# Optimization experiments

Hardware: AMD Instinct MI355X
Metric: run time of the kernel (lower is better)

Reference implementation:

```python
import jax, jax.numpy as jnp
import numpy as np

N_NODES = 65536
N_EDGES = 1048576
IN_CH, HID_CH, OUT_CH = 300, 64, 20
DROPOUT_P = 0.5


def setup_inputs() -> dict:
    key = jax.random.key(0)
    ks = jax.random.split(key, 6)
    x = jax.random.normal(ks[0], (N_NODES, IN_CH), dtype=jnp.float32)
    edge_index = jax.random.randint(ks[1], (2, N_EDGES), 0, N_NODES, dtype=jnp.int64)
    edge_weight = jax.random.uniform(ks[2], (N_EDGES,), dtype=jnp.float32)
    # Glorot-ish init for linear weights (PyG lin has no bias; GCNConv adds its own bias)
    W1 = jax.random.normal(ks[3], (IN_CH, HID_CH), dtype=jnp.float32) / np.sqrt(IN_CH)
    b1 = jnp.zeros((HID_CH,), dtype=jnp.float32)
    W2 = jax.random.normal(ks[4], (HID_CH, OUT_CH), dtype=jnp.float32) / np.sqrt(HID_CH)
    b2 = jnp.zeros((OUT_CH,), dtype=jnp.float32)
    return {"x": x, "edge_index": edge_index, "edge_weight": edge_weight,
            "W1": W1, "b1": b1, "W2": W2, "b2": b2}


def _gcn_conv(x, src, dst, edge_weight, W, b, num_nodes):
    # GCNConv with add_self_loops=False, normalize=False:
    #   h = x @ W; out[i] = sum_{e: dst(e)=i} w_e * h[src(e)]; out += b
    h = x @ W                                   # [N, C_out]
    msg = h[src] * edge_weight[:, None]         # [E, C_out]
    agg = jax.ops.segment_sum(msg, dst, num_segments=num_nodes)
    return agg + b


def reference(x, edge_index, edge_weight, W1, b1, W2, b2):
    num_nodes = x.shape[0]
    src, dst = edge_index[0], edge_index[1]
    h = _gcn_conv(x, src, dst, edge_weight, W1, b1, num_nodes)
    h = jax.nn.relu(h)
    # dropout p=0.5, training=True, deterministic fixed key
    keep = jax.random.bernoulli(jax.random.key(42), 1.0 - DROPOUT_P, h.shape)
    h = jnp.where(keep, h / (1.0 - DROPOUT_P), 0.0)
    out = _gcn_conv(h, src, dst, edge_weight, W2, b2, num_nodes)
    return out
```

## Files before the change

kernel.cpp:

```cpp
#include <hip/hip_runtime.h>

#define N_NODES 65536
#define N_EDGES 1048576
#define NB 256
#define CAP 4608
#define EPB_A 4096
#define BLK_A (N_EDGES / EPB_A)
#define EPT_A (EPB_A / 256)

typedef __attribute__((ext_vector_type(8))) short short8v;
typedef __attribute__((ext_vector_type(4))) float float4v;

__device__ __forceinline__ unsigned short f2bf(float f) {
  unsigned u = __float_as_uint(f);
  unsigned r = u + 0x7FFFu + ((u >> 16) & 1u);
  return (unsigned short)(r >> 16);
}
__device__ __forceinline__ float bflo(unsigned u) { return __uint_as_float(u << 16); }
__device__ __forceinline__ float bfhi(unsigned u) { return __uint_as_float(u & 0xFFFF0000u); }

__device__ __forceinline__ bool keep_mask(unsigned idx) {
  const unsigned k0 = 0u, k1 = 42u;
  const unsigned k2 = 0x1BD11BDAu ^ k0 ^ k1;
  unsigned x0 = 0u;
  unsigned x1 = idx;
  x0 += k0; x1 += k1;
#define TF_ROUND(r) { x0 += x1; x1 = (x1 << (r)) | (x1 >> (32 - (r))); x1 ^= x0; }
  TF_ROUND(13) TF_ROUND(15) TF_ROUND(26) TF_ROUND(6)
  x0 += k1; x1 += k2 + 1u;
  TF_ROUND(17) TF_ROUND(29) TF_ROUND(16) TF_ROUND(24)
  x0 += k2; x1 += k0 + 2u;
  TF_ROUND(13) TF_ROUND(15) TF_ROUND(26) TF_ROUND(6)
  x0 += k0; x1 += k1 + 3u;
  TF_ROUND(17) TF_ROUND(29) TF_ROUND(16) TF_ROUND(24)
  x0 += k1; x1 += k2 + 4u;
  TF_ROUND(13) TF_ROUND(15) TF_ROUND(26) TF_ROUND(6)
  x0 += k2; x1 += k0 + 5u;
#undef TF_ROUND
  return ((x0 ^ x1) & 0x80000000u) == 0u;
}

__global__ __launch_bounds__(256) void prep_w1(const float* __restrict__ W1,
                                               unsigned short* __restrict__ Wt,
                                               unsigned* __restrict__ gcur) {
  if (blockIdx.x == 0) gcur[threadIdx.x] = 0u;
  int i = blockIdx.x * 256 + threadIdx.x;
  if (i >= 64 * 320) return;
  int ch = i / 320, k = i % 320;
  float v = (k < 300) ? W1[k * 64 + ch] : 0.0f;
  Wt[i] = f2bf(v);
}

__global__ __launch_bounds__(256) void bin_pass(const int* __restrict__ ei,
                                                const float* __restrict__ ew,
                                                unsigned* __restrict__ gcur,
                                                uint2* __restrict__ binned) {
  __shared__ unsigned cnt[NB], lofs[NB], lcur[NB], gbase[NB];
  __shared__ uint2 stage[EPB_A];
  const int t = threadIdx.x;
  const int e0 = blockIdx.x * EPB_A;
  cnt[t] = 0u;
  lcur[t] = 0u;
  __syncthreads();
  unsigned pk[EPT_A], pw[EPT_A];
#pragma unroll
  for (int j = 0; j < EPT_A; ++j) {
    int e = e0 + t + j * 256;
    unsigned s = (unsigned)ei[e];
    unsigned d = (unsigned)ei[N_EDGES + e];
    pk[j] = s | (d << 16);
    pw[j] = __float_as_uint(ew[e]);
    atomicAdd(&cnt[d >> 8], 1u);
  }
  __syncthreads();
  lofs[t] = cnt[t];
  __syncthreads();
  for (int d = 1; d < NB; d <<= 1) {
    unsigned u = (t >= d) ? lofs[t - d] : 0u;
    __syncthreads();
    lofs[t] += u;
    __syncthreads();
  }
  unsigned incl = lofs[t];
  lofs[t] = incl - cnt[t];
  gbase[t] = (unsigned)t * CAP + atomicAdd(&gcur[t], cnt[t]);
  __syncthreads();
#pragma unroll
  for (int j = 0; j < EPT_A; ++j) {
    unsigned b = pk[j] >> 24;
    unsigned slot = lofs[b] + atomicAdd(&lcur[b], 1u);
    stage[slot] = make_uint2(pk[j], pw[j]);
  }
  __syncthreads();
  for (int s = t; s < EPB_A; s += 256) {
    uint2 u = stage[s];
    unsigned b = u.x >> 24;
    binned[gbase[b] + ((unsigned)s - lofs[b])] = u;
  }
}

__global__ __launch_bounds__(256) void bucket_sort(const unsigned* __restrict__ gcur,
                                                   const uint2* __restrict__ binned,
                                                   unsigned* __restrict__ sortedc,
                                                   unsigned* __restrict__ offs_p) {
  __shared__ uint2 eLDS[CAP];
  __shared__ unsigned cnt[NB], cur[NB];
  const int t = threadIdx.x;
  const int b = blockIdx.x;
  const unsigned lo = (unsigned)b * CAP;
  const unsigned n_edges = gcur[b];
  cnt[t] = 0u;
  __syncthreads();
  for (unsigned i = t; i < n_edges; i += 256) {
    uint2 u = binned[lo + i];
    eLDS[i] = u;
    atomicAdd(&cnt[(u.x >> 16) & 255u], 1u);
  }
  __syncthreads();
  cur[t] = cnt[t];
  __syncthreads();
  for (int d = 1; d < NB; d <<= 1) {
    unsigned u = (t >= d) ? cur[t - d] : 0u;
    __syncthreads();
    cur[t] += u;
    __syncthreads();
  }
  unsigned excl = cur[t] - cnt[t];
  offs_p[b * NB + t] = (lo + excl) | (cnt[t] << 21);
  __syncthreads();
  cur[t] = excl;
  __syncthreads();
  for (unsigned i = t; i < n_edges; i += 256) {
    uint2 u = eLDS[i];
    unsigned lo8 = (u.x >> 16) & 255u;
    unsigned p = lo + atomicAdd(&cur[lo8], 1u);
    sortedc[p] = (u.x & 0xFFFFu) | ((unsigned)f2bf(__uint_as_float(u.y)) << 16);
  }
}

__global__ __launch_bounds__(256) void gemm1_mfma(const float* __restrict__ x,
                                                  const unsigned short* __restrict__ Wt,
                                                  unsigned short* __restrict__ h1b) {
  __shared__ unsigned short As[64][72];
  __shared__ unsigned short Bs[64][72];
  const int t = threadIdx.x;
  const int node0 = blockIdx.x * 64;
  const int wave = t >> 6, lane = t & 63;
  const int quad = lane >> 4, l16 = lane & 15;
  float4v acc[4] = {{0.f,0.f,0.f,0.f},{0.f,0.f,0.f,0.f},{0.f,0.f,0.f,0.f},{0.f,0.f,0.f,0.f}};

  for (int kt = 0; kt < 5; ++kt) {
    const int k0 = kt * 64;
    for (int f = t; f < 1024; f += 256) {
      int node = f >> 4;
      int k = (f & 15) * 4;
      uint2 packed;
      if (k0 + k < 300) {
        float4 v = *(const float4*)(x + (size_t)(node0 + node) * 300 + k0 + k);
        packed.x = (unsigned)f2bf(v.x) | ((unsigned)f2bf(v.y) << 16);
        packed.y = (unsigned)f2bf(v.z) | ((unsigned)f2bf(v.w) << 16);
      } else {
        packed.x = 0u; packed.y = 0u;
      }
      *(uint2*)&As[node][k] = packed;
    }
    for (int f = t; f < 512; f += 256) {
      int ch = f >> 3;
      int kq = f & 7;
      uint4 v = *(const uint4*)(Wt + (size_t)ch * 320 + k0 + kq * 8);
      *(uint4*)&Bs[ch][kq * 8] = v;
    }
    __syncthreads();
    short8v a0 = *(const short8v*)&As[wave * 16 + l16][quad * 8];
    short8v a1 = *(const short8v*)&As[wave * 16 + l16][32 + quad * 8];
#pragma unroll
    for (int nt = 0; nt < 4; ++nt) {
      short8v b0 = *(const short8v*)&Bs[nt * 16 + l16][quad * 8];
      short8v b1 = *(const short8v*)&Bs[nt * 16 + l16][32 + quad * 8];
      acc[nt] = __builtin_amdgcn_mfma_f32_16x16x32_bf16(a0, b0, acc[nt], 0, 0, 0);
      acc[nt] = __builtin_amdgcn_mfma_f32_16x16x32_bf16(a1, b1, acc[nt], 0, 0, 0);
    }
    __syncthreads();
  }
#pragma unroll
  for (int nt = 0; nt < 4; ++nt) {
#pragma unroll
    for (int r = 0; r < 4; ++r) {
      h1b[(size_t)(node0 + wave * 16 + quad * 4 + r) * 64 + nt * 16 + l16] = f2bf(acc[nt][r]);
    }
  }
}

__global__ __launch_bounds__(256) void agg1_gemm2(const unsigned* __restrict__ offs_p,
                                                  const unsigned* __restrict__ sortedc,
                                                  const unsigned short* __restrict__ h1b,
                                                  const float* __restrict__ b1,
                                                  const float* __restrict__ W2,
                                                  unsigned* __restrict__ g32u) {
  __shared__ float h2[16][68];
  __shared__ float w2t[20][68];
  const int t = threadIdx.x;
  const int node0 = blockIdx.x * 16;
  for (int i = t; i < 64 * 20; i += 256) {
    w2t[i % 20][i / 20] = W2[i];
  }
  const int n = t >> 4, cg = t & 15;
  const int node = node0 + n;
  const unsigned op = offs_p[node];
  const unsigned s = op & 0x1FFFFFu;
  const unsigned e_end = s + (op >> 21);
  float4 acc = *(const float4*)(b1 + cg * 4);
  unsigned i = s;
  for (; i + 8 <= e_end; i += 8) {
    unsigned e0 = sortedc[i],     e1 = sortedc[i + 1], e2 = sortedc[i + 2], e3 = sortedc[i + 3];
    unsigned e4 = sortedc[i + 4], e5 = sortedc[i + 5], e6 = sortedc[i + 6], e7 = sortedc[i + 7];
    uint2 v0 = *(const uint2*)(h1b + ((size_t)(e0 & 0xFFFFu)) * 64 + cg * 4);
    uint2 v1 = *(const uint2*)(h1b + ((size_t)(e1 & 0xFFFFu)) * 64 + cg * 4);
    uint2 v2 = *(const uint2*)(h1b + ((size_t)(e2 & 0xFFFFu)) * 64 + cg * 4);
    uint2 v3 = *(const uint2*)(h1b + ((size_t)(e3 & 0xFFFFu)) * 64 + cg * 4);
    uint2 v4 = *(const uint2*)(h1b + ((size_t)(e4 & 0xFFFFu)) * 64 + cg * 4);
    uint2 v5 = *(const uint2*)(h1b + ((size_t)(e5 & 0xFFFFu)) * 64 + cg * 4);
    uint2 v6 = *(const uint2*)(h1b + ((size_t)(e6 & 0xFFFFu)) * 64 + cg * 4);
    uint2 v7 = *(const uint2*)(h1b + ((size_t)(e7 & 0xFFFFu)) * 64 + cg * 4);
    float w0 = bfhi(e0), w1 = bfhi(e1), w2 = bfhi(e2), w3 = bfhi(e3);
    float w4 = bfhi(e4), w5 = bfhi(e5), w6 = bfhi(e6), w7 = bfhi(e7);
    acc.x = fmaf(w0, bflo(v0.x), acc.x); acc.y = fmaf(w0, bfhi(v0.x), acc.y);
    acc.z = fmaf(w0, bflo(v0.y), acc.z); acc.w = fmaf(w0, bfhi(v0.y), acc.w);
    acc.x = fmaf(w1, bflo(v1.x), acc.x); acc.y = fmaf(w1, bfhi(v1.x), acc.y);
    acc.z = fmaf(w1, bflo(v1.y), acc.z); acc.w = fmaf(w1, bfhi(v1.y), acc.w);
    acc.x = fmaf(w2, bflo(v2.x), acc.x); acc.y = fmaf(w2, bfhi(v2.x), acc.y);
    acc.z = fmaf(w2, bflo(v2.y), acc.z); acc.w = fmaf(w2, bfhi(v2.y), acc.w);
    acc.x = fmaf(w3, bflo(v3.x), acc.x); acc.y = fmaf(w3, bfhi(v3.x), acc.y);
    acc.z = fmaf(w3, bflo(v3.y), acc.z); acc.w = fmaf(w3, bfhi(v3.y), acc.w);
    acc.x = fmaf(w4, bflo(v4.x), acc.x); acc.y = fmaf(w4, bfhi(v4.x), acc.y);
    acc.z = fmaf(w4, bflo(v4.y), acc.z); acc.w = fmaf(w4, bfhi(v4.y), acc.w);
    acc.x = fmaf(w5, bflo(v5.x), acc.x); acc.y = fmaf(w5, bfhi(v5.x), acc.y);
    acc.z = fmaf(w5, bflo(v5.y), acc.z); acc.w = fmaf(w5, bfhi(v5.y), acc.w);
    acc.x = fmaf(w6, bflo(v6.x), acc.x); acc.y = fmaf(w6, bfhi(v6.x), acc.y);
    acc.z = fmaf(w6, bflo(v6.y), acc.z); acc.w = fmaf(w6, bfhi(v6.y), acc.w);
    acc.x = fmaf(w7, bflo(v7.x), acc.x); acc.y = fmaf(w7, bfhi(v7.x), acc.y);
    acc.z = fmaf(w7, bflo(v7.y), acc.z); acc.w = fmaf(w7, bfhi(v7.y), acc.w);
  }
  for (; i < e_end; ++i) {
    unsigned e0 = sortedc[i];
    uint2 v0 = *(const uint2*)(h1b + ((size_t)(e0 & 0xFFFFu)) * 64 + cg * 4);
    float w0 = bfhi(e0);
    acc.x = fmaf(w0, bflo(v0.x), acc.x); acc.y = fmaf(w0, bfhi(v0.x), acc.y);
    acc.z = fmaf(w0, bflo(v0.y), acc.z); acc.w = fmaf(w0, bfhi(v0.y), acc.w);
  }
  const unsigned gi = (unsigned)node * 64u + (unsigned)cg * 4u;
  float r[4] = {acc.x, acc.y, acc.z, acc.w};
#pragma unroll
  for (int j = 0; j < 4; ++j) {
    float v = fmaxf(r[j], 0.0f);
    h2[n][cg * 4 + j] = keep_mask(gi + j) ? v * 2.0f : 0.0f;
  }
  __syncthreads();
  float d0 = 0.0f, d1 = 0.0f;
  if (cg < 10) {
    const int c0 = cg * 2, c1 = cg * 2 + 1;
#pragma unroll
    for (int k = 0; k < 64; k += 4) {
      float4 hv = *(const float4*)(&h2[n][k]);
      float4 w0 = *(const float4*)(&w2t[c0][k]);
      float4 w1 = *(const float4*)(&w2t[c1][k]);
      d0 = fmaf(hv.x, w0.x, d0); d0 = fmaf(hv.y, w0.y, d0);
      d0 = fmaf(hv.z, w0.z, d0); d0 = fmaf(hv.w, w0.w, d0);
      d1 = fmaf(hv.x, w1.x, d1); d1 = fmaf(hv.y, w1.y, d1);
      d1 = fmaf(hv.z, w1.z, d1); d1 = fmaf(hv.w, w1.w, d1);
    }
  }
  unsigned packed = (cg < 10) ? ((unsigned)f2bf(d0) | ((unsigned)f2bf(d1) << 16)) : 0u;
  g32u[(size_t)node * 16 + cg] = packed;
}

__global__ __launch_bounds__(256) void aggregate2(const unsigned* __restrict__ offs_p,
                                                  const unsigned* __restrict__ sortedc,
                                                  const unsigned* __restrict__ g32u,
                                                  const float* __restrict__ b2,
                                                  float* __restrict__ out) {
  const int t = threadIdx.x;
  const int n = blockIdx.x * 16 + (t >> 4);
  const int cg = t & 15;
  const unsigned op = offs_p[n];
  const unsigned s = op & 0x1FFFFFu;
  const unsigned e_end = s + (op >> 21);
  float ax = 0.0f, ay = 0.0f;
  unsigned i = s;
  for (; i + 8 <= e_end; i += 8) {
    unsigned e0 = sortedc[i],     e1 = sortedc[i + 1], e2 = sortedc[i + 2], e3 = sortedc[i + 3];
    unsigned e4 = sortedc[i + 4], e5 = sortedc[i + 5], e6 = sortedc[i + 6], e7 = sortedc[i + 7];
    unsigned v0 = g32u[(size_t)(e0 & 0xFFFFu) * 16 + cg];
    unsigned v1 = g32u[(size_t)(e1 & 0xFFFFu) * 16 + cg];
    unsigned v2 = g32u[(size_t)(e2 & 0xFFFFu) * 16 + cg];
    unsigned v3 = g32u[(size_t)(e3 & 0xFFFFu) * 16 + cg];
    unsigned v4 = g32u[(size_t)(e4 & 0xFFFFu) * 16 + cg];
    unsigned v5 = g32u[(size_t)(e5 & 0xFFFFu) * 16 + cg];
    unsigned v6 = g32u[(size_t)(e6 & 0xFFFFu) * 16 + cg];
    unsigned v7 = g32u[(size_t)(e7 & 0xFFFFu) * 16 + cg];
    float w0 = bfhi(e0), w1 = bfhi(e1), w2 = bfhi(e2), w3 = bfhi(e3);
    float w4 = bfhi(e4), w5 = bfhi(e5), w6 = bfhi(e6), w7 = bfhi(e7);
    ax = fmaf(w0, bflo(v0), ax); ay = fmaf(w0, bfhi(v0), ay);
    ax = fmaf(w1, bflo(v1), ax); ay = fmaf(w1, bfhi(v1), ay);
    ax = fmaf(w2, bflo(v2), ax); ay = fmaf(w2, bfhi(v2), ay);
    ax = fmaf(w3, bflo(v3), ax); ay = fmaf(w3, bfhi(v3), ay);
    ax = fmaf(w4, bflo(v4), ax); ay = fmaf(w4, bfhi(v4), ay);
    ax = fmaf(w5, bflo(v5), ax); ay = fmaf(w5, bfhi(v5), ay);
    ax = fmaf(w6, bflo(v6), ax); ay = fmaf(w6, bfhi(v6), ay);
    ax = fmaf(w7, bflo(v7), ax); ay = fmaf(w7, bfhi(v7), ay);
  }
  for (; i < e_end; ++i) {
    unsigned e0 = sortedc[i];
    unsigned v0 = g32u[(size_t)(e0 & 0xFFFFu) * 16 + cg];
    float w0 = bfhi(e0);
    ax = fmaf(w0, bflo(v0), ax); ay = fmaf(w0, bfhi(v0), ay);
  }
  if (cg < 10) {
    float2 o = make_float2(ax + b2[cg * 2], ay + b2[cg * 2 + 1]);
    *(float2*)(out + (size_t)n * 20 + cg * 2) = o;
  }
}

extern "C" void kernel_launch(void* const* d_in, const int* in_sizes, int n_in,
                              void* d_out, int out_size, void* d_ws, size_t ws_size,
                              hipStream_t stream) {
  const float* x  = (const float*)d_in[0];
  const int*   ei = (const int*)d_in[1];
  const float* ew = (const float*)d_in[2];
  const float* W1 = (const float*)d_in[3];
  const float* b1 = (const float*)d_in[4];
  const float* W2 = (const float*)d_in[5];
  const float* b2 = (const float*)d_in[6];
  float* out = (float*)d_out;

  unsigned short* h1b     = (unsigned short*)d_ws;
  unsigned*       g32u    = (unsigned*)(h1b + (size_t)N_NODES * 64);
  uint2*          binned  = (uint2*)(g32u + (size_t)N_NODES * 16);
  unsigned*       sortedc = (unsigned*)(binned + (size_t)NB * CAP);
  unsigned*       offs_p  = sortedc + (size_t)NB * CAP;
  unsigned short* Wt      = (unsigned short*)(offs_p + N_NODES);
  unsigned*       gcur    = (unsigned*)(Wt + 64 * 320);

  prep_w1<<<(64 * 320 + 255) / 256, 256, 0, stream>>>(W1, Wt, gcur);
  bin_pass<<<BLK_A, 256, 0, stream>>>(ei, ew, gcur, binned);
  bucket_sort<<<NB, 256, 0, stream>>>(gcur, binned, sortedc, offs_p);
  gemm1_mfma<<<N_NODES / 64, 256, 0, stream>>>(x, Wt, h1b);
  agg1_gemm2<<<N_NODES / 16, 256, 0, stream>>>(offs_p, sortedc, h1b, b1, W2, g32u);
  aggregate2<<<N_NODES / 16, 256, 0, stream>>>(offs_p, sortedc, g32u, b2, out);
}
```

Before: 223.0 us.

## Merge bucket sort and GEMM1 into one launch; use nontemporal edge loads

Measured after the change: 232.4 us. 4.2% more time.

```diff
diff --git a/kernel.cpp b/kernel.cpp
--- a/kernel.cpp
+++ b/kernel.cpp
@@ -99,94 +99,106 @@
   }
 }
 
-__global__ __launch_bounds__(256) void bucket_sort(const unsigned* __restrict__ gcur,
-                                                   const uint2* __restrict__ binned,
-                                                   unsigned* __restrict__ sortedc,
-                                                   unsigned* __restrict__ offs_p) {
-  __shared__ uint2 eLDS[CAP];
-  __shared__ unsigned cnt[NB], cur[NB];
-  const int t = threadIdx.x;
-  const int b = blockIdx.x;
-  const unsigned lo = (unsigned)b * CAP;
-  const unsigned n_edges = gcur[b];
-  cnt[t] = 0u;
-  __syncthreads();
-  for (unsigned i = t; i < n_edges; i += 256) {
-    uint2 u = binned[lo + i];
-    eLDS[i] = u;
-    atomicAdd(&cnt[(u.x >> 16) & 255u], 1u);
-  }
-  __syncthreads();
-  cur[t] = cnt[t];
-  __syncthreads();
-  for (int d = 1; d < NB; d <<= 1) {
-    unsigned u = (t >= d) ? cur[t - d] : 0u;
-    __syncthreads();
-    cur[t] += u;
-    __syncthreads();
-  }
-  unsigned excl = cur[t] - cnt[t];
-  offs_p[b * NB + t] = (lo + excl) | (cnt[t] << 21);
-  __syncthreads();
-  cur[t] = excl;
-  __syncthreads();
-  for (unsigned i = t; i < n_edges; i += 256) {
-    uint2 u = eLDS[i];
-    unsigned lo8 = (u.x >> 16) & 255u;
-    unsigned p = lo + atomicAdd(&cur[lo8], 1u);
-    sortedc[p] = (u.x & 0xFFFFu) | ((unsigned)f2bf(__uint_as_float(u.y)) << 16);
-  }
-}
-
-__global__ __launch_bounds__(256) void gemm1_mfma(const float* __restrict__ x,
+union SortGemmLDS {
+  struct {
+    unsigned long long e[CAP];
+    unsigned cnt[NB], cur[NB];
+  } bs;
+  struct {
+    unsigned short As[64][72];
+    unsigned short Bs[64][72];
+  } g1;
+};
+
+__global__ __launch_bounds__(256) void sort_gemm1(const unsigned* __restrict__ gcur,
+                                                  const uint2* __restrict__ binned,
+                                                  unsigned* __restrict__ sortedc,
+                                                  unsigned* __restrict__ offs_p,
+                                                  const float* __restrict__ x,
                                                   const unsigned short* __restrict__ Wt,
                                                   unsigned short* __restrict__ h1b) {
-  __shared__ unsigned short As[64][72];
-  __shared__ unsigned short Bs[64][72];
+  __shared__ SortGemmLDS sh;
   const int t = threadIdx.x;
-  const int node0 = blockIdx.x * 64;
-  const int wave = t >> 6, lane = t & 63;
-  const int quad = lane >> 4, l16 = lane & 15;
-  float4v acc[4] = {{0.f,0.f,0.f,0.f},{0.f,0.f,0.f,0.f},{0.f,0.f,0.f,0.f},{0.f,0.f,0.f,0.f}};
-
-  for (int kt = 0; kt < 5; ++kt) {
-    const int k0 = kt * 64;
-    for (int f = t; f < 1024; f += 256) {
-      int node = f >> 4;
-      int k = (f & 15) * 4;
-      uint2 packed;
-      if (k0 + k < 300) {
-        float4 v = *(const float4*)(x + (size_t)(node0 + node) * 300 + k0 + k);
-        packed.x = (unsigned)f2bf(v.x) | ((unsigned)f2bf(v.y) << 16);
-        packed.y = (unsigned)f2bf(v.z) | ((unsigned)f2bf(v.w) << 16);
-      } else {
-        packed.x = 0u; packed.y = 0u;
+
+  if (blockIdx.x < NB) {
+    const int b = blockIdx.x;
+    const unsigned lo = (unsigned)b * CAP;
+    const unsigned n_edges = gcur[b];
+    const unsigned long long* bin64 = (const unsigned long long*)binned;
+    sh.bs.cnt[t] = 0u;
+    __syncthreads();
+    for (unsigned i = t; i < n_edges; i += 256) {
+      unsigned long long u = __builtin_nontemporal_load(&bin64[lo + i]);
+      sh.bs.e[i] = u;
+      atomicAdd(&sh.bs.cnt[((unsigned)u >> 16) & 255u], 1u);
+    }
+    __syncthreads();
+    sh.bs.cur[t] = sh.bs.cnt[t];
+    __syncthreads();
+    for (int d = 1; d < NB; d <<= 1) {
+      unsigned u = (t >= d) ? sh.bs.cur[t - d] : 0u;
+      __syncthreads();
+      sh.bs.cur[t] += u;
+      __syncthreads();
+    }
+    unsigned excl = sh.bs.cur[t] - sh.bs.cnt[t];
+    offs_p[b * NB + t] = (lo + excl) | (sh.bs.cnt[t] << 21);
+    __syncthreads();
+    sh.bs.cur[t] = excl;
+    __syncthreads();
+    for (unsigned i = t; i < n_edges; i += 256) {
+      unsigned long long u = sh.bs.e[i];
+      unsigned key = (unsigned)u;
+      unsigned wbits = (unsigned)(u >> 32);
+      unsigned lo8 = (key >> 16) & 255u;
+      unsigned p = lo + atomicAdd(&sh.bs.cur[lo8], 1u);
+      sortedc[p] = (key & 0xFFFFu) | ((unsigned)f2bf(__uint_as_float(wbits)) << 16);
+    }
+  } else {
+    const int node0 = (blockIdx.x - NB) * 64;
+    const int wave = t >> 6, lane = t & 63;
+    const int quad = lane >> 4, l16 = lane & 15;
+    float4v acc[4] = {{0.f,0.f,0.f,0.f},{0.f,0.f,0.f,0.f},{0.f,0.f,0.f,0.f},{0.f,0.f,0.f,0.f}};
+
+    for (int kt = 0; kt < 5; ++kt) {
+      const int k0 = kt * 64;
+      for (int f = t; f < 1024; f += 256) {
+        int node = f >> 4;
+        int k = (f & 15) * 4;
+        uint2 packed;
+        if (k0 + k < 300) {
+          float4 v = *(const float4*)(x + (size_t)(node0 + node) * 300 + k0 + k);
+          packed.x = (unsigned)f2bf(v.x) | ((unsigned)f2bf(v.y) << 16);
+          packed.y = (unsigned)f2bf(v.z) | ((unsigned)f2bf(v.w) << 16);
+        } else {
+          packed.x = 0u; packed.y = 0u;
+        }
+        *(uint2*)&sh.g1.As[node][k] = packed;
       }
-      *(uint2*)&As[node][k] = packed;
-    }
-    for (int f = t; f < 512; f += 256) {
-      int ch = f >> 3;
-      int kq = f & 7;
-      uint4 v = *(const uint4*)(Wt + (size_t)ch * 320 + k0 + kq * 8);
-      *(uint4*)&Bs[ch][kq * 8] = v;
-    }
-    __syncthreads();
-    short8v a0 = *(const short8v*)&As[wave * 16 + l16][quad * 8];
-    short8v a1 = *(const short8v*)&As[wave * 16 + l16][32 + quad * 8];
+      for (int f = t; f < 512; f += 256) {
+        int ch = f >> 3;
+        int kq = f & 7;
+        uint4 v = *(const uint4*)(Wt + (size_t)ch * 320 + k0 + kq * 8);
+        *(uint4*)&sh.g1.Bs[ch][kq * 8] = v;
+      }
+      __syncthreads();
+      short8v a0 = *(const short8v*)&sh.g1.As[wave * 16 + l16][quad * 8];
+      short8v a1 = *(const short8v*)&sh.g1.As[wave * 16 + l16][32 + quad * 8];
+#pragma unroll
+      for (int nt = 0; nt < 4; ++nt) {
+        short8v b0 = *(const short8v*)&sh.g1.Bs[nt * 16 + l16][quad * 8];
+        short8v b1 = *(const short8v*)&sh.g1.Bs[nt * 16 + l16][32 + quad * 8];
+        acc[nt] = __builtin_amdgcn_mfma_f32_16x16x32_bf16(a0, b0, acc[nt], 0, 0, 0);
+        acc[nt] = __builtin_amdgcn_mfma_f32_16x16x32_bf16(a1, b1, acc[nt], 0, 0, 0);
+      }
+      __syncthreads();
+    }
 #pragma unroll
     for (int nt = 0; nt < 4; ++nt) {
-      short8v b0 = *(const short8v*)&Bs[nt * 16 + l16][quad * 8];
-      short8v b1 = *(const short8v*)&Bs[nt * 16 + l16][32 + quad * 8];
-      acc[nt] = __builtin_amdgcn_mfma_f32_16x16x32_bf16(a0, b0, acc[nt], 0, 0, 0);
-      acc[nt] = __builtin_amdgcn_mfma_f32_16x16x32_bf16(a1, b1, acc[nt], 0, 0, 0);
-    }
-    __syncthreads();
-  }
-#pragma unroll
-  for (int nt = 0; nt < 4; ++nt) {
-#pragma unroll
-    for (int r = 0; r < 4; ++r) {
-      h1b[(size_t)(node0 + wave * 16 + quad * 4 + r) * 64 + nt * 16 + l16] = f2bf(acc[nt][r]);
+#pragma unroll
+      for (int r = 0; r < 4; ++r) {
+        h1b[(size_t)(node0 + wave * 16 + quad * 4 + r) * 64 + nt * 16 + l16] = f2bf(acc[nt][r]);
+      }
     }
   }
 }
@@ -212,8 +224,14 @@
   float4 acc = *(const float4*)(b1 + cg * 4);
   unsigned i = s;
   for (; i + 8 <= e_end; i += 8) {
-    unsigned e0 = sortedc[i],     e1 = sortedc[i + 1], e2 = sortedc[i + 2], e3 = sortedc[i + 3];
-    unsigned e4 = sortedc[i + 4], e5 = sortedc[i + 5], e6 = sortedc[i + 6], e7 = sortedc[i + 7];
+    unsigned e0 = __builtin_nontemporal_load(&sortedc[i]);
+    unsigned e1 = __builtin_nontemporal_load(&sortedc[i + 1]);
+    unsigned e2 = __builtin_nontemporal_load(&sortedc[i + 2]);
+    unsigned e3 = __builtin_nontemporal_load(&sortedc[i + 3]);
+    unsigned e4 = __builtin_nontemporal_load(&sortedc[i + 4]);
+    unsigned e5 = __builtin_nontemporal_load(&sortedc[i + 5]);
+    unsigned e6 = __builtin_nontemporal_load(&sortedc[i + 6]);
+    unsigned e7 = __builtin_nontemporal_load(&sortedc[i + 7]);
     uint2 v0 = *(const uint2*)(h1b + ((size_t)(e0 & 0xFFFFu)) * 64 + cg * 4);
     uint2 v1 = *(const uint2*)(h1b + ((size_t)(e1 & 0xFFFFu)) * 64 + cg * 4);
     uint2 v2 = *(const uint2*)(h1b + ((size_t)(e2 & 0xFFFFu)) * 64 + cg * 4);
@@ -242,7 +260,7 @@
     acc.z = fmaf(w7, bflo(v7.y), acc.z); acc.w = fmaf(w7, bfhi(v7.y), acc.w);
   }
   for (; i < e_end; ++i) {
-    unsigned e0 = sortedc[i];
+    unsigned e0 = __builtin_nontemporal_load(&sortedc[i]);
     uint2 v0 = *(const uint2*)(h1b + ((size_t)(e0 & 0xFFFFu)) * 64 + cg * 4);
     float w0 = bfhi(e0);
     acc.x = fmaf(w0, bflo(v0.x), acc.x); acc.y = fmaf(w0, bfhi(v0.x), acc.y);
@@ -288,8 +306,14 @@
   float ax = 0.0f, ay = 0.0f;
   unsigned i = s;
   for (; i + 8 <= e_end; i += 8) {
-    unsigned e0 = sortedc[i],     e1 = sortedc[i + 1], e2 = sortedc[i + 2], e3 = sortedc[i + 3];
-    unsigned e4 = sortedc[i + 4], e5 = sortedc[i + 5], e6 = sortedc[i + 6], e7 = sortedc[i + 7];
+    unsigned e0 = __builtin_nontemporal_load(&sortedc[i]);
+    unsigned e1 = __builtin_nontemporal_load(&sortedc[i + 1]);
+    unsigned e2 = __builtin_nontemporal_load(&sortedc[i + 2]);
+    unsigned e3 = __builtin_nontemporal_load(&sortedc[i + 3]);
+    unsigned e4 = __builtin_nontemporal_load(&sortedc[i + 4]);
+    unsigned e5 = __builtin_nontemporal_load(&sortedc[i + 5]);
+    unsigned e6 = __builtin_nontemporal_load(&sortedc[i + 6]);
+    unsigned e7 = __builtin_nontemporal_load(&sortedc[i + 7]);
     unsigned v0 = g32u[(size_t)(e0 & 0xFFFFu) * 16 + cg];
     unsigned v1 = g32u[(size_t)(e1 & 0xFFFFu) * 16 + cg];
     unsigned v2 = g32u[(size_t)(e2 & 0xFFFFu) * 16 + cg];
@@ -310,7 +334,7 @@
     ax = fmaf(w7, bflo(v7), ax); ay = fmaf(w7, bfhi(v7), ay);
   }
   for (; i < e_end; ++i) {
-    unsigned e0 = sortedc[i];
+    unsigned e0 = __builtin_nontemporal_load(&sortedc[i]);
     unsigned v0 = g32u[(size_t)(e0 & 0xFFFFu) * 16 + cg];
     float w0 = bfhi(e0);
     ax = fmaf(w0, bflo(v0), ax); ay = fmaf(w0, bfhi(v0), ay);
@@ -343,8 +367,7 @@
 
   prep_w1<<<(64 * 320 + 255) / 256, 256, 0, stream>>>(W1, Wt, gcur);
   bin_pass<<<BLK_A, 256, 0, stream>>>(ei, ew, gcur, binned);
-  bucket_sort<<<NB, 256, 0, stream>>>(gcur, binned, sortedc, offs_p);
-  gemm1_mfma<<<N_NODES / 64, 256, 0, stream>>>(x, Wt, h1b);
+  sort_gemm1<<<NB + N_NODES / 64, 256, 0, stream>>>(gcur, binned, sortedc, offs_p, x, Wt, h1b);
   agg1_gemm2<<<N_NODES / 16, 256, 0, stream>>>(offs_p, sortedc, h1b, b1, W2, g32u);
   aggregate2<<<N_NODES / 16, 256, 0, stream>>>(offs_p, sortedc, g32u, b2, out);
 }
```
